# Performance work log

Hardware: AMD Instinct MI355X
Metric: run time of the kernel (lower is better)

The kernel has to match this reference:

```python
import jax, jax.numpy as jnp
import numpy as np

B, H, S, D = 2, 8, 4096, 64
TEMPERATURE = 8.0


def setup_inputs() -> dict:
    key = jax.random.key(0)
    kq, kk, kv, km = jax.random.split(key, 4)
    q = jax.random.normal(kq, (B, H, S, D), dtype=jnp.float32)
    k = jax.random.normal(kk, (B, H, S, D), dtype=jnp.float32)
    v = jax.random.normal(kv, (B, H, S, D), dtype=jnp.float32)
    mask = jax.random.randint(km, (1, 1, S, S), 0, 2, dtype=jnp.int32)
    return {"q": q, "k": k, "v": v, "mask": mask}


def reference(q, k, v, mask):
    # scores = q @ k^T / temperature  -> [B,H,S,S]
    scores = jnp.einsum("bhqd,bhkd->bhqk", q, k) / TEMPERATURE
    # masked_fill(mask == 0, -inf)
    scores = jnp.where(mask == 0, -jnp.inf, scores)
    attn = jax.nn.softmax(scores, axis=-1)
    output = jnp.einsum("bhqk,bhkd->bhqd", attn, v)
    return (output, attn)
```

## Files before the change

kernel.cpp:

```cpp
#include <hip/hip_runtime.h>
#include <stdint.h>

typedef __attribute__((ext_vector_type(8))) short short8;
typedef __attribute__((ext_vector_type(4))) float float4v;

#define SEQ 4096
#define HD 64
#define QB 128
#define KT 64
#define HEADS 16
#define NT (SEQ / KT)
#define MWORDS (SEQ / 64)
#define TILE_BYTES 8192
#define QSCALE 0.18033688f

__device__ __forceinline__ ushort f2bf(float f) {
    union { float f; uint32_t u; } x; x.f = f;
    uint32_t u = x.u;
    return (ushort)((u + 0x7FFFu + ((u >> 16) & 1u)) >> 16);
}

__device__ __forceinline__ uint32_t cvt_pk_bf16(float lo, float hi) {
    uint32_t r;
    asm("v_cvt_pk_bf16_f32 %0, %1, %2" : "=v"(r) : "v"(lo), "v"(hi));
    return r;
}

__device__ __forceinline__ float exp2_hw(float x) { return __builtin_amdgcn_exp2f(x); }
__device__ __forceinline__ float log2_hw(float x) { return __builtin_amdgcn_logf(x); }

__device__ __forceinline__ void gload_lds16(const void* g, void* l) {
    __builtin_amdgcn_global_load_lds(
        (const __attribute__((address_space(1))) uint32_t*)g,
        (__attribute__((address_space(3))) uint32_t*)l, 16, 0, 0);
}

__global__ __launch_bounds__(256) void pack_mask_kernel(const int* __restrict__ mask,
                                                        unsigned long long* __restrict__ mb) {
    const int qrow = blockIdx.x;
    const int wave = threadIdx.x >> 6;
    const int lane = threadIdx.x & 63;
    const int* rp = mask + (size_t)qrow * SEQ;
    #pragma unroll
    for (int i = 0; i < 16; ++i) {
        const int widx = wave * 16 + i;
        const int mv = rp[widx * 64 + lane];
        unsigned long long b = __ballot(mv != 0);
        if (lane == 0) mb[(size_t)qrow * MWORDS + widx] = b;
    }
}

__global__ __launch_bounds__(256) void prep_kv_kernel(const float* __restrict__ kg,
                                                      const float* __restrict__ vg,
                                                      char* __restrict__ ktiles,
                                                      char* __restrict__ vtiles) {
    __shared__ __align__(16) float Tl[64][68];
    const int bid = blockIdx.x;
    const int tid = threadIdx.x;
    const float* Kg = kg + (size_t)bid * KT * HD;
    const float* Vg = vg + (size_t)bid * KT * HD;
    char* Kt = ktiles + (size_t)bid * TILE_BYTES;
    char* Vt = vtiles + (size_t)bid * TILE_BYTES;

    {
        const int r = tid >> 2, c0 = (tid & 3) * 16;
        #pragma unroll
        for (int j = 0; j < 4; ++j)
            *(float4v*)&Tl[r][c0 + j * 4] = *(const float4v*)(Kg + r * HD + c0 + j * 4);
    }
    __syncthreads();
    #pragma unroll
    for (int cc = 0; cc < 2; ++cc) {
        const int c = tid + cc * 256;
        const int t = c >> 7, h = (c >> 6) & 1, g = (c >> 4) & 3, li = c & 15;
        const int row = 32 * (t >> 1) + 8 * (li >> 2) + 4 * (t & 1) + (li & 3);
        const float* src = &Tl[row][h * 32 + g * 8];
        short8 w;
        #pragma unroll
        for (int e = 0; e < 8; ++e) w[e] = (short)f2bf(src[e]);
        *(short8*)(Kt + c * 16) = w;
    }
    __syncthreads();
    {
        const int r = tid >> 2, c0 = (tid & 3) * 16;
        #pragma unroll
        for (int j = 0; j < 4; ++j)
            *(float4v*)&Tl[r][c0 + j * 4] = *(const float4v*)(Vg + r * HD + c0 + j * 4);
    }
    __syncthreads();
    #pragma unroll
    for (int cc = 0; cc < 2; ++cc) {
        const int c = tid + cc * 256;
        const int dt = c >> 7, h = (c >> 6) & 1, g = (c >> 4) & 3, li = c & 15;
        short8 w;
        #pragma unroll
        for (int e = 0; e < 8; ++e) w[e] = (short)f2bf(Tl[h * 32 + g * 8 + e][dt * 16 + li]);
        *(short8*)(Vt + c * 16) = w;
    }
}

#define STAGE_K(KTI, DST) do {                                                     \
    const char* _s = Ktile + (size_t)(KTI) * TILE_BYTES + wave * 1024 + lane * 16; \
    gload_lds16(_s, (char*)(DST) + wave * 1024);                                   \
} while (0)

#define STAGE_V(KTI, DST) do {                                                     \
    const char* _s = Vtile + (size_t)(KTI) * TILE_BYTES + wave * 1024 + lane * 16; \
    gload_lds16(_s, (char*)(DST) + wave * 1024);                                   \
} while (0)

__global__ __launch_bounds__(512, 4) void attn_kernel(
    const float* __restrict__ qg, const unsigned long long* __restrict__ mb,
    const char* __restrict__ ktiles, const char* __restrict__ vtiles,
    float* __restrict__ outg, float* __restrict__ attng)
{
    __shared__ __align__(16) char Lds[4][TILE_BYTES];

    const int tid  = threadIdx.x;
    const int wave = tid >> 6;
    const int lane = tid & 63;
    const int g    = lane >> 4;
    const int li   = lane & 15;

    const int bid = blockIdx.x;
    const int blk = (bid & 7) * 64 + (bid >> 3);
    const int bh  = blk >> 5;
    const int qb  = blk & 31;

    const size_t qkvBase = (size_t)bh * SEQ * HD;
    const float* Qg = qg + qkvBase + (size_t)qb * QB * HD;
    const char* Ktile = ktiles + (size_t)bh * NT * TILE_BYTES;
    const char* Vtile = vtiles + (size_t)bh * NT * TILE_BYTES;

    const int wq0 = wave * 16;
    short8 aq[2];
    #pragma unroll
    for (int h = 0; h < 2; ++h) {
        const float* src = Qg + (wq0 + li) * HD + h * 32 + g * 8;
        short8 t;
        #pragma unroll
        for (int e = 0; e < 8; ++e) t[e] = (short)f2bf(src[e] * QSCALE);
        aq[h] = t;
    }

    const int qrow = qb * QB + wq0 + li;
    const unsigned long long* mrow = mb + (size_t)qrow * MWORDS;

    STAGE_K(0, Lds[0]);
    STAGE_K(1, Lds[1]);
    asm volatile("s_waitcnt vmcnt(1)" ::: "memory");
    __builtin_amdgcn_s_barrier();
    asm volatile("" ::: "memory");

    float lsum = 0.f;
    for (int kt = 0; kt < NT; ++kt) {
        const unsigned long long mw = mrow[kt];
        __builtin_amdgcn_sched_barrier(0);
        if (kt + 2 < NT) STAGE_K(kt + 2, Lds[(kt + 2) % 3]);
        __builtin_amdgcn_sched_barrier(0);
        const uint32_t mlo = (uint32_t)mw >> (g * 8);
        const uint32_t mhi = (uint32_t)(mw >> 32) >> (g * 8);

        const char* Kb = Lds[kt % 3] + lane * 16;
        short8 bk[4][2];
        #pragma unroll
        for (int t = 0; t < 4; ++t)
            #pragma unroll
            for (int h = 0; h < 2; ++h)
                bk[t][h] = *(const short8*)(Kb + (t * 2 + h) * 1024);

        float4v accs[4];
        #pragma unroll
        for (int t = 0; t < 4; ++t) accs[t] = (float4v){0.f, 0.f, 0.f, 0.f};
        __builtin_amdgcn_s_setprio(1);
        #pragma unroll
        for (int t = 0; t < 4; ++t) {
            accs[t] = __builtin_amdgcn_mfma_f32_16x16x32_bf16(bk[t][0], aq[0], accs[t], 0, 0, 0);
            accs[t] = __builtin_amdgcn_mfma_f32_16x16x32_bf16(bk[t][1], aq[1], accs[t], 0, 0, 0);
        }
        __builtin_amdgcn_s_setprio(0);
        const uint32_t nib[4] = { mlo & 0xFu, (mlo >> 4) & 0xFu, mhi & 0xFu, (mhi >> 4) & 0xFu };
        #pragma unroll
        for (int t = 0; t < 4; ++t) {
            #pragma unroll
            for (int r = 0; r < 4; ++r) {
                const float e = exp2_hw(accs[t][r]);
                lsum += ((nib[t] >> r) & 1u) ? e : 0.f;
            }
        }
        if (kt < NT - 2) {
            asm volatile("s_waitcnt vmcnt(1)" ::: "memory");
            __builtin_amdgcn_s_barrier();
            asm volatile("" ::: "memory");
        } else if (kt == NT - 2) {
            asm volatile("s_waitcnt vmcnt(0)" ::: "memory");
            __builtin_amdgcn_s_barrier();
            asm volatile("" ::: "memory");
        }
    }
    lsum += __shfl_xor(lsum, 16);
    lsum += __shfl_xor(lsum, 32);
    const float linv2 = -log2_hw(lsum);

    float* attnT = attng + (size_t)bh * SEQ * SEQ + (size_t)qrow * SEQ + g * 8;
    float4v acco[4];
    #pragma unroll
    for (int dt = 0; dt < 4; ++dt) acco[dt] = (float4v){0.f, 0.f, 0.f, 0.f};

    __syncthreads();
    STAGE_K(0, Lds[0]);
    STAGE_V(0, Lds[2]);
    asm volatile("s_waitcnt vmcnt(0)" ::: "memory");
    __builtin_amdgcn_s_barrier();
    asm volatile("" ::: "memory");

    for (int kt = 0; kt < NT; ++kt) {
        const int b = kt & 1;
        const unsigned long long mw = mrow[kt];
        __builtin_amdgcn_sched_barrier(0);
        if (kt < NT - 1) { STAGE_K(kt + 1, Lds[b ^ 1]); STAGE_V(kt + 1, Lds[2 + (b ^ 1)]); }
        __builtin_amdgcn_sched_barrier(0);

        const uint32_t mlo = (uint32_t)mw >> (g * 8);
        const uint32_t mhi = (uint32_t)(mw >> 32) >> (g * 8);

        const char* Kb = Lds[b] + lane * 16;
        const char* Vb = Lds[2 + b] + lane * 16;
        short8 bk[4][2], vb[4][2];
        #pragma unroll
        for (int t = 0; t < 4; ++t)
            #pragma unroll
            for (int h = 0; h < 2; ++h) {
                bk[t][h] = *(const short8*)(Kb + (t * 2 + h) * 1024);
                vb[t][h] = *(const short8*)(Vb + (t * 2 + h) * 1024);
            }

        float4v accs[4];
        #pragma unroll
        for (int t = 0; t < 4; ++t) accs[t] = (float4v){0.f, 0.f, 0.f, 0.f};
        __builtin_amdgcn_s_setprio(1);
        #pragma unroll
        for (int t = 0; t < 4; ++t) {
            accs[t] = __builtin_amdgcn_mfma_f32_16x16x32_bf16(bk[t][0], aq[0], accs[t], 0, 0, 0);
            accs[t] = __builtin_amdgcn_mfma_f32_16x16x32_bf16(bk[t][1], aq[1], accs[t], 0, 0, 0);
        }
        __builtin_amdgcn_s_setprio(0);

        const uint32_t nib[4] = { mlo & 0xFu, (mlo >> 4) & 0xFu, mhi & 0xFu, (mhi >> 4) & 0xFu };
        float4v pv[4];
        #pragma unroll
        for (int t = 0; t < 4; ++t) {
            #pragma unroll
            for (int r = 0; r < 4; ++r) {
                const float e = exp2_hw(accs[t][r] + linv2);
                pv[t][r] = ((nib[t] >> r) & 1u) ? e : 0.f;
            }
        }

        uint32_t pk[4][2];
        #pragma unroll
        for (int t = 0; t < 4; ++t) {
            pk[t][0] = cvt_pk_bf16(pv[t][0], pv[t][1]);
            pk[t][1] = cvt_pk_bf16(pv[t][2], pv[t][3]);
        }
        union { uint32_t u[4]; short8 s; } pa0, pa1;
        pa0.u[0] = pk[0][0]; pa0.u[1] = pk[0][1]; pa0.u[2] = pk[1][0]; pa0.u[3] = pk[1][1];
        pa1.u[0] = pk[2][0]; pa1.u[1] = pk[2][1]; pa1.u[2] = pk[3][0]; pa1.u[3] = pk[3][1];

        __builtin_amdgcn_s_setprio(1);
        #pragma unroll
        for (int dt = 0; dt < 4; ++dt) {
            acco[dt] = __builtin_amdgcn_mfma_f32_16x16x32_bf16(vb[dt][0], pa0.s, acco[dt], 0, 0, 0);
            acco[dt] = __builtin_amdgcn_mfma_f32_16x16x32_bf16(vb[dt][1], pa1.s, acco[dt], 0, 0, 0);
        }
        __builtin_amdgcn_s_setprio(0);

        float* ap = attnT + kt * KT;
        *(float4v*)(ap)      = pv[0];
        *(float4v*)(ap + 4)  = pv[1];
        *(float4v*)(ap + 32) = pv[2];
        *(float4v*)(ap + 36) = pv[3];

        if (kt < NT - 1) {
            asm volatile("s_waitcnt vmcnt(4)" ::: "memory");
            __builtin_amdgcn_s_barrier();
            asm volatile("" ::: "memory");
        }
    }

    float* outW = outg + qkvBase + (size_t)qrow * HD + g * 4;
    #pragma unroll
    for (int dt = 0; dt < 4; ++dt) {
        *(float4v*)(outW + dt * 16) = acco[dt];
    }
}

extern "C" void kernel_launch(void* const* d_in, const int* in_sizes, int n_in,
                              void* d_out, int out_size, void* d_ws, size_t ws_size,
                              hipStream_t stream) {
    (void)in_sizes; (void)n_in; (void)out_size; (void)ws_size;
    const float* q = (const float*)d_in[0];
    const float* k = (const float*)d_in[1];
    const float* v = (const float*)d_in[2];
    const int* mask = (const int*)d_in[3];

    float* outp  = (float*)d_out;
    float* attnp = outp + (size_t)2 * 8 * SEQ * HD;

    char* ws = (char*)d_ws;
    unsigned long long* mb = (unsigned long long*)ws;
    char* ktiles = ws + (size_t)2 * 1024 * 1024;
    char* vtiles = ws + (size_t)10 * 1024 * 1024;

    pack_mask_kernel<<<SEQ, 256, 0, stream>>>(mask, mb);
    prep_kv_kernel<<<HEADS * NT, 256, 0, stream>>>(k, v, ktiles, vtiles);
    attn_kernel<<<HEADS * (SEQ / QB), 512, 0, stream>>>(q, mb, ktiles, vtiles, outp, attnp);
}
```

Measured before the change: 411.3 us.

## Process two key tiles per barrier step with deeper LDS prefetch in both passes

Both attention passes now handle a pair of 64-key tiles per barrier step instead of one. The first pass prefetches two tiles ahead into a six-slot K ring, and the second pass double-buffers K/V tile pairs. Mask words for the next pair are loaded one iteration early, and attention-row stores are issued before the PV MFMAs. This halves barrier count and deepens prefetch, but LDS per block grows from 32KB to 64KB, which may cut resident blocks per CU under the 512x4 launch bounds.

```diff
diff --git a/kernel.cpp b/kernel.cpp
--- a/kernel.cpp
+++ b/kernel.cpp
@@ -10,6 +10,7 @@
 #define KT 64
 #define HEADS 16
 #define NT (SEQ / KT)
+#define NTP (NT / 2)
 #define MWORDS (SEQ / 64)
 #define TILE_BYTES 8192
 #define QSCALE 0.18033688f
@@ -114,7 +115,7 @@
     const char* __restrict__ ktiles, const char* __restrict__ vtiles,
     float* __restrict__ outg, float* __restrict__ attng)
 {
-    __shared__ __align__(16) char Lds[4][TILE_BYTES];
+    __shared__ __align__(16) char Lds[8][TILE_BYTES];
 
     const int tid  = threadIdx.x;
     const int wave = tid >> 6;
@@ -146,29 +147,15 @@
     const int qrow = qb * QB + wq0 + li;
     const unsigned long long* mrow = mb + (size_t)qrow * MWORDS;
 
-    STAGE_K(0, Lds[0]);
-    STAGE_K(1, Lds[1]);
-    asm volatile("s_waitcnt vmcnt(1)" ::: "memory");
-    __builtin_amdgcn_s_barrier();
-    asm volatile("" ::: "memory");
-
     float lsum = 0.f;
-    for (int kt = 0; kt < NT; ++kt) {
-        const unsigned long long mw = mrow[kt];
-        __builtin_amdgcn_sched_barrier(0);
-        if (kt + 2 < NT) STAGE_K(kt + 2, Lds[(kt + 2) % 3]);
-        __builtin_amdgcn_sched_barrier(0);
-        const uint32_t mlo = (uint32_t)mw >> (g * 8);
-        const uint32_t mhi = (uint32_t)(mw >> 32) >> (g * 8);
-
-        const char* Kb = Lds[kt % 3] + lane * 16;
+    auto sub1 = [&](const char* Kb0, unsigned long long mw) {
+        const char* Kb = Kb0 + lane * 16;
         short8 bk[4][2];
         #pragma unroll
         for (int t = 0; t < 4; ++t)
             #pragma unroll
             for (int h = 0; h < 2; ++h)
                 bk[t][h] = *(const short8*)(Kb + (t * 2 + h) * 1024);
-
         float4v accs[4];
         #pragma unroll
         for (int t = 0; t < 4; ++t) accs[t] = (float4v){0.f, 0.f, 0.f, 0.f};
@@ -179,24 +166,48 @@
             accs[t] = __builtin_amdgcn_mfma_f32_16x16x32_bf16(bk[t][1], aq[1], accs[t], 0, 0, 0);
         }
         __builtin_amdgcn_s_setprio(0);
+        const uint32_t mlo = (uint32_t)mw >> (g * 8);
+        const uint32_t mhi = (uint32_t)(mw >> 32) >> (g * 8);
         const uint32_t nib[4] = { mlo & 0xFu, (mlo >> 4) & 0xFu, mhi & 0xFu, (mhi >> 4) & 0xFu };
         #pragma unroll
-        for (int t = 0; t < 4; ++t) {
+        for (int t = 0; t < 4; ++t)
             #pragma unroll
             for (int r = 0; r < 4; ++r) {
                 const float e = exp2_hw(accs[t][r]);
                 lsum += ((nib[t] >> r) & 1u) ? e : 0.f;
             }
-        }
-        if (kt < NT - 2) {
-            asm volatile("s_waitcnt vmcnt(1)" ::: "memory");
+    };
+
+    unsigned long long mwA = mrow[0], mwB = mrow[1];
+    __builtin_amdgcn_sched_barrier(0);
+    STAGE_K(0, Lds[0]); STAGE_K(1, Lds[1]);
+    STAGE_K(2, Lds[2]); STAGE_K(3, Lds[3]);
+    asm volatile("s_waitcnt vmcnt(2)" ::: "memory");
+    __builtin_amdgcn_s_barrier();
+    asm volatile("" ::: "memory");
+
+    for (int p = 0; p < NTP; ++p) {
+        if (p + 2 < NTP) {
+            STAGE_K(2 * p + 4, Lds[(2 * p + 4) % 6]);
+            STAGE_K(2 * p + 5, Lds[(2 * p + 5) % 6]);
+        }
+        unsigned long long mwAn = 0, mwBn = 0;
+        if (p + 1 < NTP) { mwAn = mrow[2 * p + 2]; mwBn = mrow[2 * p + 3]; }
+        __builtin_amdgcn_sched_barrier(0);
+
+        sub1(Lds[(2 * p) % 6], mwA);
+        sub1(Lds[(2 * p + 1) % 6], mwB);
+
+        if (p < NTP - 2) {
+            asm volatile("s_waitcnt vmcnt(4)" ::: "memory");
             __builtin_amdgcn_s_barrier();
             asm volatile("" ::: "memory");
-        } else if (kt == NT - 2) {
-            asm volatile("s_waitcnt vmcnt(0)" ::: "memory");
+        } else if (p == NTP - 2) {
+            asm volatile("s_waitcnt vmcnt(2)" ::: "memory");
             __builtin_amdgcn_s_barrier();
             asm volatile("" ::: "memory");
         }
+        mwA = mwAn; mwB = mwBn;
     }
     lsum += __shfl_xor(lsum, 16);
     lsum += __shfl_xor(lsum, 32);
@@ -207,25 +218,9 @@
     #pragma unroll
     for (int dt = 0; dt < 4; ++dt) acco[dt] = (float4v){0.f, 0.f, 0.f, 0.f};
 
-    __syncthreads();
-    STAGE_K(0, Lds[0]);
-    STAGE_V(0, Lds[2]);
-    asm volatile("s_waitcnt vmcnt(0)" ::: "memory");
-    __builtin_amdgcn_s_barrier();
-    asm volatile("" ::: "memory");
-
-    for (int kt = 0; kt < NT; ++kt) {
-        const int b = kt & 1;
-        const unsigned long long mw = mrow[kt];
-        __builtin_amdgcn_sched_barrier(0);
-        if (kt < NT - 1) { STAGE_K(kt + 1, Lds[b ^ 1]); STAGE_V(kt + 1, Lds[2 + (b ^ 1)]); }
-        __builtin_amdgcn_sched_barrier(0);
-
-        const uint32_t mlo = (uint32_t)mw >> (g * 8);
-        const uint32_t mhi = (uint32_t)(mw >> 32) >> (g * 8);
-
-        const char* Kb = Lds[b] + lane * 16;
-        const char* Vb = Lds[2 + b] + lane * 16;
+    auto sub2 = [&](const char* Kb0, const char* Vb0, unsigned long long mw, int kt) {
+        const char* Kb = Kb0 + lane * 16;
+        const char* Vb = Vb0 + lane * 16;
         short8 bk[4][2], vb[4][2];
         #pragma unroll
         for (int t = 0; t < 4; ++t)
@@ -234,7 +229,6 @@
                 bk[t][h] = *(const short8*)(Kb + (t * 2 + h) * 1024);
                 vb[t][h] = *(const short8*)(Vb + (t * 2 + h) * 1024);
             }
-
         float4v accs[4];
         #pragma unroll
         for (int t = 0; t < 4; ++t) accs[t] = (float4v){0.f, 0.f, 0.f, 0.f};
@@ -246,34 +240,17 @@
         }
         __builtin_amdgcn_s_setprio(0);
 
+        const uint32_t mlo = (uint32_t)mw >> (g * 8);
+        const uint32_t mhi = (uint32_t)(mw >> 32) >> (g * 8);
         const uint32_t nib[4] = { mlo & 0xFu, (mlo >> 4) & 0xFu, mhi & 0xFu, (mhi >> 4) & 0xFu };
         float4v pv[4];
         #pragma unroll
-        for (int t = 0; t < 4; ++t) {
+        for (int t = 0; t < 4; ++t)
             #pragma unroll
             for (int r = 0; r < 4; ++r) {
                 const float e = exp2_hw(accs[t][r] + linv2);
                 pv[t][r] = ((nib[t] >> r) & 1u) ? e : 0.f;
             }
-        }
-
-        uint32_t pk[4][2];
-        #pragma unroll
-        for (int t = 0; t < 4; ++t) {
-            pk[t][0] = cvt_pk_bf16(pv[t][0], pv[t][1]);
-            pk[t][1] = cvt_pk_bf16(pv[t][2], pv[t][3]);
-        }
-        union { uint32_t u[4]; short8 s; } pa0, pa1;
-        pa0.u[0] = pk[0][0]; pa0.u[1] = pk[0][1]; pa0.u[2] = pk[1][0]; pa0.u[3] = pk[1][1];
-        pa1.u[0] = pk[2][0]; pa1.u[1] = pk[2][1]; pa1.u[2] = pk[3][0]; pa1.u[3] = pk[3][1];
-
-        __builtin_amdgcn_s_setprio(1);
-        #pragma unroll
-        for (int dt = 0; dt < 4; ++dt) {
-            acco[dt] = __builtin_amdgcn_mfma_f32_16x16x32_bf16(vb[dt][0], pa0.s, acco[dt], 0, 0, 0);
-            acco[dt] = __builtin_amdgcn_mfma_f32_16x16x32_bf16(vb[dt][1], pa1.s, acco[dt], 0, 0, 0);
-        }
-        __builtin_amdgcn_s_setprio(0);
 
         float* ap = attnT + kt * KT;
         *(float4v*)(ap)      = pv[0];
@@ -281,11 +258,54 @@
         *(float4v*)(ap + 32) = pv[2];
         *(float4v*)(ap + 36) = pv[3];
 
-        if (kt < NT - 1) {
-            asm volatile("s_waitcnt vmcnt(4)" ::: "memory");
+        uint32_t pk[4][2];
+        #pragma unroll
+        for (int t = 0; t < 4; ++t) {
+            pk[t][0] = cvt_pk_bf16(pv[t][0], pv[t][1]);
+            pk[t][1] = cvt_pk_bf16(pv[t][2], pv[t][3]);
+        }
+        union { uint32_t u[4]; short8 s; } pa0, pa1;
+        pa0.u[0] = pk[0][0]; pa0.u[1] = pk[0][1]; pa0.u[2] = pk[1][0]; pa0.u[3] = pk[1][1];
+        pa1.u[0] = pk[2][0]; pa1.u[1] = pk[2][1]; pa1.u[2] = pk[3][0]; pa1.u[3] = pk[3][1];
+
+        __builtin_amdgcn_s_setprio(1);
+        #pragma unroll
+        for (int dt = 0; dt < 4; ++dt) {
+            acco[dt] = __builtin_amdgcn_mfma_f32_16x16x32_bf16(vb[dt][0], pa0.s, acco[dt], 0, 0, 0);
+            acco[dt] = __builtin_amdgcn_mfma_f32_16x16x32_bf16(vb[dt][1], pa1.s, acco[dt], 0, 0, 0);
+        }
+        __builtin_amdgcn_s_setprio(0);
+    };
+
+    __syncthreads();
+    mwA = mrow[0]; mwB = mrow[1];
+    __builtin_amdgcn_sched_barrier(0);
+    STAGE_K(0, Lds[0]); STAGE_K(1, Lds[1]);
+    STAGE_V(0, Lds[2]); STAGE_V(1, Lds[3]);
+    asm volatile("s_waitcnt vmcnt(0)" ::: "memory");
+    __builtin_amdgcn_s_barrier();
+    asm volatile("" ::: "memory");
+
+    for (int p = 0; p < NTP; ++p) {
+        const int gb = (p & 1) << 2;
+        const int gn = gb ^ 4;
+        if (p + 1 < NTP) {
+            STAGE_K(2 * p + 2, Lds[gn + 0]); STAGE_K(2 * p + 3, Lds[gn + 1]);
+            STAGE_V(2 * p + 2, Lds[gn + 2]); STAGE_V(2 * p + 3, Lds[gn + 3]);
+        }
+        unsigned long long mwAn = 0, mwBn = 0;
+        if (p + 1 < NTP) { mwAn = mrow[2 * p + 2]; mwBn = mrow[2 * p + 3]; }
+        __builtin_amdgcn_sched_barrier(0);
+
+        sub2(Lds[gb + 0], Lds[gb + 2], mwA, 2 * p);
+        sub2(Lds[gb + 1], Lds[gb + 3], mwB, 2 * p + 1);
+
+        if (p < NTP - 1) {
+            asm volatile("s_waitcnt vmcnt(8)" ::: "memory");
             __builtin_amdgcn_s_barrier();
             asm volatile("" ::: "memory");
         }
+        mwA = mwAn; mwB = mwBn;
     }
 
     float* outW = outg + qkvBase + (size_t)qrow * HD + g * 4;
```

New measurement: 400.8 us. -2.6%, faster.
